# Optimization experiments

Hardware: AMD Instinct MI355X
Metric: run time of the kernel (lower is better)

Reference implementation:

```python
import jax, jax.numpy as jnp
import numpy as np

P = 16        # patch size
WIN = 64      # attention window size
NH = 12       # num heads


def _layernorm(x, g, b, eps=1e-5):
    m = x.mean(-1, keepdims=True)
    v = ((x - m) ** 2).mean(-1, keepdims=True)
    return (x - m) * jax.lax.rsqrt(v + eps) * g + b


def _sinusoidal_pe(n, d):
    pos = jnp.arange(n, dtype=jnp.float32)[:, None]
    i = jnp.arange(d // 2, dtype=jnp.float32)[None, :]
    ang = pos / jnp.power(10000.0, (2.0 * i) / d)
    pe = jnp.zeros((n, d), jnp.float32)
    pe = pe.at[:, 0::2].set(jnp.sin(ang)).at[:, 1::2].set(jnp.cos(ang))
    return pe


def setup_inputs() -> dict:
    key = jax.random.key(0)
    ks = jax.random.split(key, 8)
    B, C, H, W, D, F = 16, 3, 512, 512, 768, 3072
    s = lambda k, shape: (jax.random.normal(k, shape, jnp.float32) * 0.02)
    return {
        "input": jax.random.normal(ks[0], (B, C, H, W), jnp.float32),
        "patch_w": s(ks[1], (D, C, P, P)),
        "patch_b": jnp.zeros((D,), jnp.float32),
        "ln_g": jnp.ones((D,), jnp.float32),
        "ln_b": jnp.zeros((D,), jnp.float32),
        "qkv_w": s(ks[2], (D, 3 * D)),
        "qkv_b": jnp.zeros((3 * D,), jnp.float32),
        "proj_w": s(ks[3], (D, D)),
        "proj_b": jnp.zeros((D,), jnp.float32),
        "ff1_w": s(ks[4], (D, F)),
        "ff1_b": jnp.zeros((F,), jnp.float32),
        "ff2_w": s(ks[5], (F, D)),
        "ff2_b": jnp.zeros((D,), jnp.float32),
    }


def reference(input, patch_w, patch_b, ln_g, ln_b, qkv_w, qkv_b,
              proj_w, proj_b, ff1_w, ff1_b, ff2_w, ff2_b):
    B, C, H, W = input.shape
    D = patch_w.shape[0]
    dh = D // NH
    # --- patch embedding (conv k=stride=P as einsum) + norm ---
    xp = input.reshape(B, C, H // P, P, W // P, P)
    x = jnp.einsum('bchpwq,dcpq->bhwd', xp, patch_w) + patch_b  # [B,32,32,D]
    x = x.reshape(B, -1, D)                                      # [B,N,D]
    x = _layernorm(x, ln_g, ln_b)
    N = x.shape[1]
    # --- static sinusoidal position embedding ---
    x = x + _sinusoidal_pe(N, D)

    def ff(y):  # shared feedforward (dropout=eval/off)
        return jax.nn.gelu(y @ ff1_w + ff1_b) @ ff2_w + ff2_b

    def sparse_attn(y):  # windowed block-sparse attention, window=64
        nW = N // WIN
        qkv = (y @ qkv_w + qkv_b).reshape(B, nW, WIN, 3, NH, dh)
        q, k, v = qkv[:, :, :, 0], qkv[:, :, :, 1], qkv[:, :, :, 2]
        scores = jnp.einsum('bwqhd,bwkhd->bwhqk', q, k) * (dh ** -0.5)
        a = jax.nn.softmax(scores, axis=-1)
        o = jnp.einsum('bwhqk,bwkhd->bwqhd', a, v).reshape(B, N, D)
        return o @ proj_w + proj_b

    identity = x
    x = ff(x)
    x = sparse_attn(x)
    x = x + identity
    identity = x
    x = ff(x)
    x = x + identity
    return x
```

## Files before the change

### kernel.cpp

```cpp
#include <hip/hip_runtime.h>

typedef unsigned int uint;
typedef short bf16x8 __attribute__((ext_vector_type(8)));
typedef float f32x4 __attribute__((ext_vector_type(4)));

__device__ __forceinline__ unsigned short f2b(float f) {
    uint u = __builtin_bit_cast(uint, f);
    u += 0x7fffu + ((u >> 16) & 1u);
    return (unsigned short)(u >> 16);
}
__device__ __forceinline__ float b2f(unsigned short h) {
    uint u = ((uint)h) << 16;
    return __builtin_bit_cast(float, u);
}

__device__ __forceinline__ float fast_gelu(float v) {
    float s  = v * v;
    float t2 = __builtin_fmaf(0.044715f * s, v, v);
    float e  = __expf(-1.5957691216f * t2);
    return v * __builtin_amdgcn_rcpf(1.0f + e);
}

__device__ __forceinline__ void gl_lds16(const unsigned short* g, unsigned short* l) {
    __builtin_amdgcn_global_load_lds(
        reinterpret_cast<const __attribute__((address_space(1))) unsigned int*>(
            reinterpret_cast<uintptr_t>(g)),
        reinterpret_cast<__attribute__((address_space(3))) unsigned int*>(
            reinterpret_cast<uintptr_t>(l)),
        16, 0, 0);
}

__global__ __launch_bounds__(256) void convert_bf16_kernel(const float* __restrict__ src,
                                                           unsigned short* __restrict__ dst, int n) {
    int idx = blockIdx.x * 256 + threadIdx.x;
    if (idx < n) dst[idx] = f2b(src[idx]);
}

__global__ __launch_bounds__(256) void transpose_to_bf16_kernel(const float* __restrict__ src,
                                                                unsigned short* __restrict__ dst,
                                                                int K, int N) {
    long long idx = (long long)blockIdx.x * 256 + threadIdx.x;
    if (idx >= (long long)K * N) return;
    int k = (int)(idx / N);
    int n = (int)(idx % N);
    dst[(long long)n * K + k] = f2b(src[idx]);
}

__global__ __launch_bounds__(256) void im2col_kernel(const float* __restrict__ in,
                                                     unsigned short* __restrict__ out) {
    long long idx = (long long)blockIdx.x * 256 + threadIdx.x;
    int k = (int)(idx % 768);
    int n = (int)(idx / 768);
    int b = n >> 10, t = n & 1023;
    int hp = t >> 5, wp = t & 31;
    int c = k >> 8, rm = k & 255;
    int p = rm >> 4, q = rm & 15;
    long long src = (((long long)(b * 3 + c) * 512) + hp * 16 + p) * 512 + wp * 16 + q;
    out[idx] = f2b(in[src]);
}

__global__ __launch_bounds__(256) void ln_pe_kernel(const float* __restrict__ xe,
                                                    const float* __restrict__ g,
                                                    const float* __restrict__ bb,
                                                    unsigned short* __restrict__ xb) {
    int row = blockIdx.x;
    int pos = row & 1023;
    const float* xr = xe + (long long)row * 768;
    float v0 = xr[threadIdx.x];
    float v1 = xr[threadIdx.x + 256];
    float v2 = xr[threadIdx.x + 512];
    float s = v0 + v1 + v2;
    float sq = v0 * v0 + v1 * v1 + v2 * v2;
    for (int o = 32; o > 0; o >>= 1) {
        s  += __shfl_down(s, o, 64);
        sq += __shfl_down(sq, o, 64);
    }
    __shared__ float ps[4], pq[4];
    int w = threadIdx.x >> 6, lane = threadIdx.x & 63;
    if (lane == 0) { ps[w] = s; pq[w] = sq; }
    __syncthreads();
    float ts = ps[0] + ps[1] + ps[2] + ps[3];
    float tq = pq[0] + pq[1] + pq[2] + pq[3];
    float mean = ts * (1.0f / 768.0f);
    float var  = tq * (1.0f / 768.0f) - mean * mean;
    float inv  = rsqrtf(var + 1e-5f);
    #pragma unroll
    for (int dd = 0; dd < 3; dd++) {
        int d = threadIdx.x + dd * 256;
        float val = (dd == 0) ? v0 : (dd == 1) ? v1 : v2;
        float y = (val - mean) * inv * g[d] + bb[d];
        float freq = __expf(-(float)(d & ~1) * (9.210340371976184f / 768.0f));
        float ang = (float)pos * freq;
        y += (d & 1) ? cosf(ang) : sinf(ang);
        xb[(long long)row * 768 + d] = f2b(y);
    }
}

__global__ __launch_bounds__(256) void gemm128_kernel(const unsigned short* __restrict__ A,
                                                      const unsigned short* __restrict__ BT,
                                                      const float* __restrict__ bias,
                                                      const unsigned short* __restrict__ residB,
                                                      float* __restrict__ outF,
                                                      unsigned short* __restrict__ outB,
                                                      int M, int N, int K, int ldb,
                                                      int epi, int accumF) {
    __shared__ unsigned short As[128 * 64];
    __shared__ unsigned short Bs[128 * 64];

    const int nX = N >> 7;
    int id = blockIdx.x;
    int xcd = id & 7;
    int sq_ = id >> 3;
    int bx = sq_ % nX;
    int by = (sq_ / nX) * 8 + xcd;

    const int tid = threadIdx.x;
    const int m0 = by * 128, n0 = bx * 128;
    const int w = tid >> 6, lane = tid & 63;
    const int wm = (w >> 1) * 64, wn = (w & 1) * 64;
    const int quad = lane >> 4, l15 = lane & 15;

    const int srow = tid >> 3;
    const int sc8  = tid & 7;
    const int gc8  = sc8 ^ (srow & 7);
    const unsigned short* Ag0 = A  + (long long)(m0 + srow) * K + gc8 * 8;
    const unsigned short* Ag1 = Ag0 + (long long)32 * K;
    const unsigned short* Ag2 = Ag0 + (long long)64 * K;
    const unsigned short* Ag3 = Ag0 + (long long)96 * K;
    const unsigned short* Bg0 = BT + (long long)(n0 + srow) * ldb + gc8 * 8;
    const unsigned short* Bg1 = Bg0 + (long long)32 * ldb;
    const unsigned short* Bg2 = Bg0 + (long long)64 * ldb;
    const unsigned short* Bg3 = Bg0 + (long long)96 * ldb;
    unsigned short* Ad0 = As + srow * 64 + sc8 * 8;
    unsigned short* Ad1 = Ad0 + 32 * 64;
    unsigned short* Ad2 = Ad0 + 64 * 64;
    unsigned short* Ad3 = Ad0 + 96 * 64;
    unsigned short* Bd0 = Bs + srow * 64 + sc8 * 8;
    unsigned short* Bd1 = Bd0 + 32 * 64;
    unsigned short* Bd2 = Bd0 + 64 * 64;
    unsigned short* Bd3 = Bd0 + 96 * 64;

    f32x4 acc[4][4] = {};
    const int swz = l15 & 7;

    for (int k0 = 0; k0 < K; k0 += 64) {
        __syncthreads();
        gl_lds16(Ag0 + k0, Ad0);
        gl_lds16(Ag1 + k0, Ad1);
        gl_lds16(Ag2 + k0, Ad2);
        gl_lds16(Ag3 + k0, Ad3);
        gl_lds16(Bg0 + k0, Bd0);
        gl_lds16(Bg1 + k0, Bd1);
        gl_lds16(Bg2 + k0, Bd2);
        gl_lds16(Bg3 + k0, Bd3);
        __syncthreads();

        #pragma unroll
        for (int h = 0; h < 2; h++) {
            const int c8 = h * 4 + quad;
            bf16x8 af[4], bfr[4];
            #pragma unroll
            for (int i = 0; i < 4; i++)
                af[i] = *(const bf16x8*)(As + (wm + i * 16 + l15) * 64 + ((c8 ^ swz) * 8));
            #pragma unroll
            for (int j = 0; j < 4; j++)
                bfr[j] = *(const bf16x8*)(Bs + (wn + j * 16 + l15) * 64 + ((c8 ^ swz) * 8));
            #pragma unroll
            for (int i = 0; i < 4; i++)
                #pragma unroll
                for (int j = 0; j < 4; j++)
                    acc[i][j] = __builtin_amdgcn_mfma_f32_16x16x32_bf16(af[i], bfr[j], acc[i][j], 0, 0, 0);
        }
    }

    const int r0 = quad * 4;
    #pragma unroll
    for (int i = 0; i < 4; i++) {
        #pragma unroll
        for (int j = 0; j < 4; j++) {
            int gn = n0 + wn + j * 16 + l15;
            float bv = bias ? bias[gn] : 0.0f;
            #pragma unroll
            for (int r = 0; r < 4; r++) {
                int gm = m0 + wm + i * 16 + r0 + r;
                float v = acc[i][j][r] + bv;
                if (epi == 1) v = fast_gelu(v);
                long long off = (long long)gm * N + gn;
                if (accumF) v += outF[off];
                if (residB) v += b2f(residB[off]);
                if (outF) outF[off] = v;
                if (outB) outB[off] = f2b(v);
            }
        }
    }
}

__global__ __launch_bounds__(256) void attn_kernel(const unsigned short* __restrict__ qkv,
                                                   unsigned short* __restrict__ o) {
    __shared__ float qs[64 * 65], ks[64 * 65], vs[64 * 65];
    __shared__ float pmax[4 * 64], psum[4 * 64];
    int blk = blockIdx.x;
    int h = blk % 12;
    int bw = blk / 12;
    int wi = bw % 16, b = bw / 16;
    int rowBase = b * 1024 + wi * 64;
    int tid = threadIdx.x;

    int lr = tid >> 2, c0 = (tid & 3) * 16;
    const unsigned short* src = qkv + (long long)(rowBase + lr) * 2304 + h * 64 + c0;
    #pragma unroll
    for (int j = 0; j < 16; j++) {
        qs[lr * 65 + c0 + j] = b2f(src[j]);
        ks[lr * 65 + c0 + j] = b2f(src[768 + j]);
        vs[lr * 65 + c0 + j] = b2f(src[1536 + j]);
    }
    __syncthreads();

    int r = tid & 63, cg = tid >> 6;
    float svals[16] = {};
    for (int kk = 0; kk < 64; kk++) {
        float qv = qs[r * 65 + kk];
        #pragma unroll
        for (int j = 0; j < 16; j++)
            svals[j] += qv * ks[(cg * 16 + j) * 65 + kk];
    }
    float smax = -1e30f;
    #pragma unroll
    for (int j = 0; j < 16; j++) {
        svals[j] *= 0.125f;
        smax = fmaxf(smax, svals[j]);
    }
    pmax[cg * 64 + r] = smax;
    __syncthreads();
    float m = fmaxf(fmaxf(pmax[r], pmax[64 + r]), fmaxf(pmax[128 + r], pmax[192 + r]));
    float lsum = 0.0f;
    #pragma unroll
    for (int j = 0; j < 16; j++) {
        float e = __expf(svals[j] - m);
        qs[r * 65 + cg * 16 + j] = e;
        lsum += e;
    }
    psum[cg * 64 + r] = lsum;
    __syncthreads();
    float inv = __builtin_amdgcn_rcpf(psum[r] + psum[64 + r] + psum[128 + r] + psum[192 + r]);

    float oacc[16] = {};
    for (int c = 0; c < 64; c++) {
        float pv = qs[r * 65 + c];
        #pragma unroll
        for (int j = 0; j < 16; j++)
            oacc[j] += pv * vs[c * 65 + cg * 16 + j];
    }
    unsigned short* dst = o + (long long)(rowBase + r) * 768 + h * 64 + cg * 16;
    #pragma unroll
    for (int j = 0; j < 16; j++) dst[j] = f2b(oacc[j] * inv);
}

extern "C" void kernel_launch(void* const* d_in, const int* in_sizes, int n_in,
                              void* d_out, int out_size, void* d_ws, size_t ws_size,
                              hipStream_t stream) {
    const float* input   = (const float*)d_in[0];
    const float* patch_w = (const float*)d_in[1];
    const float* patch_b = (const float*)d_in[2];
    const float* ln_g    = (const float*)d_in[3];
    const float* ln_b    = (const float*)d_in[4];
    const float* qkv_w   = (const float*)d_in[5];
    const float* qkv_b   = (const float*)d_in[6];
    const float* proj_w  = (const float*)d_in[7];
    const float* proj_b  = (const float*)d_in[8];
    const float* ff1_w   = (const float*)d_in[9];
    const float* ff1_b   = (const float*)d_in[10];
    const float* ff2_w   = (const float*)d_in[11];
    const float* ff2_b   = (const float*)d_in[12];
    float* out = (float*)d_out;

    const int MN = 16384;
    const int D = 768, F = 3072, TD = 2304;
    const int NY = MN / 128;

    unsigned short* wPatch = (unsigned short*)d_ws;
    unsigned short* wQkvT  = wPatch + 589824;
    unsigned short* wProjT = wQkvT + 1769472;
    unsigned short* wFf1T  = wProjT + 589824;
    unsigned short* wFf2T  = wFf1T + 2359296;
    unsigned short* bigBuf = wFf2T + 2359296;
    unsigned short* xid    = bigBuf + 50331648;
    unsigned short* t0     = xid + 12582912;

    convert_bf16_kernel<<<(589824 + 255) / 256, 256, 0, stream>>>(patch_w, wPatch, 589824);
    transpose_to_bf16_kernel<<<(1769472 + 255) / 256, 256, 0, stream>>>(qkv_w, wQkvT, D, TD);
    transpose_to_bf16_kernel<<<(589824 + 255) / 256, 256, 0, stream>>>(proj_w, wProjT, D, D);
    transpose_to_bf16_kernel<<<(2359296 + 255) / 256, 256, 0, stream>>>(ff1_w, wFf1T, D, F);
    transpose_to_bf16_kernel<<<(2359296 + 255) / 256, 256, 0, stream>>>(ff2_w, wFf2T, F, D);

    im2col_kernel<<<(MN * 768) / 256, 256, 0, stream>>>(input, bigBuf);

    gemm128_kernel<<<(D / 128) * NY, 256, 0, stream>>>(bigBuf, wPatch, patch_b, nullptr,
                                                       out, nullptr, MN, D, 768, 768, 0, 0);
    ln_pe_kernel<<<MN, 256, 0, stream>>>(out, ln_g, ln_b, xid);

    gemm128_kernel<<<(F / 128) * NY, 256, 0, stream>>>(xid, wFf1T, ff1_b, nullptr,
                                                       nullptr, bigBuf, MN, F, 768, 768, 1, 0);
    gemm128_kernel<<<(D / 128) * NY, 256, 0, stream>>>(bigBuf, wFf2T, ff2_b, nullptr,
                                                       nullptr, t0, MN, D, F, F, 0, 0);
    gemm128_kernel<<<(TD / 128) * NY, 256, 0, stream>>>(t0, wQkvT, qkv_b, nullptr,
                                                        nullptr, bigBuf, MN, TD, 768, 768, 0, 0);
    attn_kernel<<<16 * 16 * 12, 256, 0, stream>>>(bigBuf, t0);

    gemm128_kernel<<<(D / 128) * NY, 256, 0, stream>>>(t0, wProjT, proj_b, xid,
                                                       nullptr, xid, MN, D, 768, 768, 0, 0);

    gemm128_kernel<<<(F / 128) * NY, 256, 0, stream>>>(xid, wFf1T, ff1_b, nullptr,
                                                       nullptr, bigBuf, MN, F, 768, 768, 1, 0);
    gemm128_kernel<<<(D / 128) * NY, 256, 0, stream>>>(bigBuf, wFf2T, ff2_b, xid,
                                                       out, nullptr, MN, D, F, F, 0, 0);
}
```

Measured before the change: 900.1 us.

## Replace 128x128 GEMM with double-buffered 256x256 tile, 8-wave pipelined kernel

```diff
diff --git a/kernel.cpp b/kernel.cpp
--- a/kernel.cpp
+++ b/kernel.cpp
@@ -96,7 +96,7 @@
     }
 }
 
-__global__ __launch_bounds__(256) void gemm128_kernel(const unsigned short* __restrict__ A,
+__global__ __launch_bounds__(512) void gemm256_kernel(const unsigned short* __restrict__ A,
                                                       const unsigned short* __restrict__ BT,
                                                       const float* __restrict__ bias,
                                                       const unsigned short* __restrict__ residB,
@@ -104,95 +104,141 @@
                                                       unsigned short* __restrict__ outB,
                                                       int M, int N, int K, int ldb,
                                                       int epi, int accumF) {
-    __shared__ unsigned short As[128 * 64];
-    __shared__ unsigned short Bs[128 * 64];
-
-    const int nX = N >> 7;
+    __shared__ __align__(16) unsigned short As[2][256 * 64];
+    __shared__ __align__(16) unsigned short Bs[2][256 * 64];
+
+    const int nX = N >> 8;
     int id = blockIdx.x;
     int xcd = id & 7;
     int sq_ = id >> 3;
     int bx = sq_ % nX;
     int by = (sq_ / nX) * 8 + xcd;
+    const int m0 = by * 256, n0 = bx * 256;
 
     const int tid = threadIdx.x;
-    const int m0 = by * 128, n0 = bx * 128;
     const int w = tid >> 6, lane = tid & 63;
-    const int wm = (w >> 1) * 64, wn = (w & 1) * 64;
+    const int wr = w >> 2, wc = w & 3;
     const int quad = lane >> 4, l15 = lane & 15;
-
-    const int srow = tid >> 3;
-    const int sc8  = tid & 7;
-    const int gc8  = sc8 ^ (srow & 7);
-    const unsigned short* Ag0 = A  + (long long)(m0 + srow) * K + gc8 * 8;
-    const unsigned short* Ag1 = Ag0 + (long long)32 * K;
-    const unsigned short* Ag2 = Ag0 + (long long)64 * K;
-    const unsigned short* Ag3 = Ag0 + (long long)96 * K;
-    const unsigned short* Bg0 = BT + (long long)(n0 + srow) * ldb + gc8 * 8;
-    const unsigned short* Bg1 = Bg0 + (long long)32 * ldb;
-    const unsigned short* Bg2 = Bg0 + (long long)64 * ldb;
-    const unsigned short* Bg3 = Bg0 + (long long)96 * ldb;
-    unsigned short* Ad0 = As + srow * 64 + sc8 * 8;
-    unsigned short* Ad1 = Ad0 + 32 * 64;
-    unsigned short* Ad2 = Ad0 + 64 * 64;
-    unsigned short* Ad3 = Ad0 + 96 * 64;
-    unsigned short* Bd0 = Bs + srow * 64 + sc8 * 8;
-    unsigned short* Bd1 = Bd0 + 32 * 64;
-    unsigned short* Bd2 = Bd0 + 64 * 64;
-    unsigned short* Bd3 = Bd0 + 96 * 64;
-
-    f32x4 acc[4][4] = {};
     const int swz = l15 & 7;
 
-    for (int k0 = 0; k0 < K; k0 += 64) {
-        __syncthreads();
-        gl_lds16(Ag0 + k0, Ad0);
-        gl_lds16(Ag1 + k0, Ad1);
-        gl_lds16(Ag2 + k0, Ad2);
-        gl_lds16(Ag3 + k0, Ad3);
-        gl_lds16(Bg0 + k0, Bd0);
-        gl_lds16(Bg1 + k0, Bd1);
-        gl_lds16(Bg2 + k0, Bd2);
-        gl_lds16(Bg3 + k0, Bd3);
-        __syncthreads();
-
+    const int row0 = tid >> 3;
+    const int c8   = tid & 7;
+    const int gc8  = c8 ^ (row0 & 7);
+    const unsigned short* Ag = A  + (long long)(m0 + row0) * K   + gc8 * 8;
+    const unsigned short* Bg = BT + (long long)(n0 + row0) * ldb + gc8 * 8;
+    unsigned short* Ad = &As[0][0] + row0 * 64 + c8 * 8;
+    unsigned short* Bd = &Bs[0][0] + row0 * 64 + c8 * 8;
+    const long long aK64 = (long long)64 * K,  aK128 = (long long)128 * K;
+    const long long bL64 = (long long)64 * ldb, bL128 = (long long)128 * ldb;
+
+#define STAGE_A(bsel, h, ks) { \
+    const unsigned short* s_ = Ag + (h) * aK128 + (ks); \
+    unsigned short* d_ = Ad + (bsel) * 16384 + (h) * 8192; \
+    gl_lds16(s_, d_); gl_lds16(s_ + aK64, d_ + 4096); }
+#define STAGE_B(bsel, h, ks) { \
+    const unsigned short* s_ = Bg + (h) * bL128 + (ks); \
+    unsigned short* d_ = Bd + (bsel) * 16384 + (h) * 8192; \
+    gl_lds16(s_, d_); gl_lds16(s_ + bL64, d_ + 4096); }
+
+    bf16x8 af[4][2], bfr[2][2];
+    f32x4 acc[2][2][4][2] = {};
+
+#define LOAD_AF(bsel, qm) { \
+    const unsigned short* base_ = &As[bsel][((qm) * 128 + wr * 64 + l15) * 64]; \
+    _Pragma("unroll") for (int mf_ = 0; mf_ < 4; mf_++) { \
+      af[mf_][0] = *(const bf16x8*)(base_ + mf_ * 1024 + ((quad ^ swz) * 8)); \
+      af[mf_][1] = *(const bf16x8*)(base_ + mf_ * 1024 + (((4 + quad) ^ swz) * 8)); \
+    } }
+#define LOAD_BF(bsel, qn) { \
+    const unsigned short* base_ = &Bs[bsel][((qn) * 128 + wc * 32 + l15) * 64]; \
+    _Pragma("unroll") for (int nf_ = 0; nf_ < 2; nf_++) { \
+      bfr[nf_][0] = *(const bf16x8*)(base_ + nf_ * 1024 + ((quad ^ swz) * 8)); \
+      bfr[nf_][1] = *(const bf16x8*)(base_ + nf_ * 1024 + (((4 + quad) ^ swz) * 8)); \
+    } }
+#define MFMA_Q(qm, qn) { \
+    __builtin_amdgcn_sched_barrier(0); \
+    __builtin_amdgcn_s_setprio(1); \
+    _Pragma("unroll") for (int mf_ = 0; mf_ < 4; mf_++) \
+    _Pragma("unroll") for (int nf_ = 0; nf_ < 2; nf_++) { \
+      acc[qm][qn][mf_][nf_] = __builtin_amdgcn_mfma_f32_16x16x32_bf16(af[mf_][0], bfr[nf_][0], acc[qm][qn][mf_][nf_], 0, 0, 0); \
+      acc[qm][qn][mf_][nf_] = __builtin_amdgcn_mfma_f32_16x16x32_bf16(af[mf_][1], bfr[nf_][1], acc[qm][qn][mf_][nf_], 0, 0, 0); \
+    } \
+    __builtin_amdgcn_s_setprio(0); \
+    __builtin_amdgcn_sched_barrier(0); }
+#define BAR() { asm volatile("" ::: "memory"); __builtin_amdgcn_s_barrier(); asm volatile("" ::: "memory"); }
+
+    const int NT = K >> 6;
+
+    STAGE_B(0, 0, 0);
+    STAGE_A(0, 0, 0);
+    STAGE_B(0, 1, 0);
+    STAGE_A(0, 1, 0);
+    STAGE_A(1, 0, 64);
+    STAGE_B(1, 1, 64);
+    STAGE_A(1, 1, 64);
+    asm volatile("s_waitcnt vmcnt(6)" ::: "memory");
+    BAR();
+
+    for (int s = 0; s < NT; s++) {
+        const int b = s & 1, bn = b ^ 1;
+        const int ks1 = (s + 1 < NT) ? (s + 1) * 64 : 0;
+        const int ks2 = (s + 2 < NT) ? (s + 2) * 64 : 0;
+
+        LOAD_AF(b, 0);
+        LOAD_BF(b, 0);
+        STAGE_B(bn, 0, ks1);
+        asm volatile("s_waitcnt lgkmcnt(8)" ::: "memory");
+        BAR();
+        MFMA_Q(0, 0);
+        BAR();
+        LOAD_BF(b, 1);
+        STAGE_A(b, 0, ks2);
+        BAR();
+        MFMA_Q(0, 1);
+        BAR();
+        LOAD_AF(b, 1);
+        STAGE_B(b, 1, ks2);
+        BAR();
+        MFMA_Q(1, 1);
+        BAR();
+        LOAD_BF(b, 0);
+        STAGE_A(b, 1, ks2);
+        BAR();
+        MFMA_Q(1, 0);
+        asm volatile("s_waitcnt vmcnt(6)" ::: "memory");
+        BAR();
+    }
+    asm volatile("s_waitcnt vmcnt(0)" ::: "memory");
+
+    const int r0 = quad * 4;
+    #pragma unroll
+    for (int qm = 0; qm < 2; qm++)
+    #pragma unroll
+    for (int qn = 0; qn < 2; qn++)
+    #pragma unroll
+    for (int mf = 0; mf < 4; mf++)
+    #pragma unroll
+    for (int nf = 0; nf < 2; nf++) {
+        int gn = n0 + qn * 128 + wc * 32 + nf * 16 + l15;
+        float bv = bias ? bias[gn] : 0.0f;
         #pragma unroll
-        for (int h = 0; h < 2; h++) {
-            const int c8 = h * 4 + quad;
-            bf16x8 af[4], bfr[4];
-            #pragma unroll
-            for (int i = 0; i < 4; i++)
-                af[i] = *(const bf16x8*)(As + (wm + i * 16 + l15) * 64 + ((c8 ^ swz) * 8));
-            #pragma unroll
-            for (int j = 0; j < 4; j++)
-                bfr[j] = *(const bf16x8*)(Bs + (wn + j * 16 + l15) * 64 + ((c8 ^ swz) * 8));
-            #pragma unroll
-            for (int i = 0; i < 4; i++)
-                #pragma unroll
-                for (int j = 0; j < 4; j++)
-                    acc[i][j] = __builtin_amdgcn_mfma_f32_16x16x32_bf16(af[i], bfr[j], acc[i][j], 0, 0, 0);
+        for (int r = 0; r < 4; r++) {
+            int gm = m0 + qm * 128 + wr * 64 + mf * 16 + r0 + r;
+            float v = acc[qm][qn][mf][nf][r] + bv;
+            if (epi == 1) v = fast_gelu(v);
+            long long off = (long long)gm * N + gn;
+            if (accumF) v += outF[off];
+            if (residB) v += b2f(residB[off]);
+            if (outF) outF[off] = v;
+            if (outB) outB[off] = f2b(v);
         }
     }
-
-    const int r0 = quad * 4;
-    #pragma unroll
-    for (int i = 0; i < 4; i++) {
-        #pragma unroll
-        for (int j = 0; j < 4; j++) {
-            int gn = n0 + wn + j * 16 + l15;
-            float bv = bias ? bias[gn] : 0.0f;
-            #pragma unroll
-            for (int r = 0; r < 4; r++) {
-                int gm = m0 + wm + i * 16 + r0 + r;
-                float v = acc[i][j][r] + bv;
-                if (epi == 1) v = fast_gelu(v);
-                long long off = (long long)gm * N + gn;
-                if (accumF) v += outF[off];
-                if (residB) v += b2f(residB[off]);
-                if (outF) outF[off] = v;
-                if (outB) outB[off] = f2b(v);
-            }
-        }
-    }
+#undef STAGE_A
+#undef STAGE_B
+#undef LOAD_AF
+#undef LOAD_BF
+#undef MFMA_Q
+#undef BAR
 }
 
 __global__ __launch_bounds__(256) void attn_kernel(const unsigned short* __restrict__ qkv,
@@ -276,7 +322,7 @@
 
     const int MN = 16384;
     const int D = 768, F = 3072, TD = 2304;
-    const int NY = MN / 128;
+    const int NY = MN / 256;
 
     unsigned short* wPatch = (unsigned short*)d_ws;
     unsigned short* wQkvT  = wPatch + 589824;
@@ -295,23 +341,23 @@
 
     im2col_kernel<<<(MN * 768) / 256, 256, 0, stream>>>(input, bigBuf);
 
-    gemm128_kernel<<<(D / 128) * NY, 256, 0, stream>>>(bigBuf, wPatch, patch_b, nullptr,
+    gemm256_kernel<<<(D / 256) * NY, 512, 0, stream>>>(bigBuf, wPatch, patch_b, nullptr,
                                                        out, nullptr, MN, D, 768, 768, 0, 0);
     ln_pe_kernel<<<MN, 256, 0, stream>>>(out, ln_g, ln_b, xid);
 
-    gemm128_kernel<<<(F / 128) * NY, 256, 0, stream>>>(xid, wFf1T, ff1_b, nullptr,
+    gemm256_kernel<<<(F / 256) * NY, 512, 0, stream>>>(xid, wFf1T, ff1_b, nullptr,
                                                        nullptr, bigBuf, MN, F, 768, 768, 1, 0);
-    gemm128_kernel<<<(D / 128) * NY, 256, 0, stream>>>(bigBuf, wFf2T, ff2_b, nullptr,
+    gemm256_kernel<<<(D / 256) * NY, 512, 0, stream>>>(bigBuf, wFf2T, ff2_b, nullptr,
                                                        nullptr, t0, MN, D, F, F, 0, 0);
-    gemm128_kernel<<<(TD / 128) * NY, 256, 0, stream>>>(t0, wQkvT, qkv_b, nullptr,
+    gemm256_kernel<<<(TD / 256) * NY, 512, 0, stream>>>(t0, wQkvT, qkv_b, nullptr,
                                                         nullptr, bigBuf, MN, TD, 768, 768, 0, 0);
     attn_kernel<<<16 * 16 * 12, 256, 0, stream>>>(bigBuf, t0);
 
-    gemm128_kernel<<<(D / 128) * NY, 256, 0, stream>>>(t0, wProjT, proj_b, xid,
+    gemm256_kernel<<<(D / 256) * NY, 512, 0, stream>>>(t0, wProjT, proj_b, xid,
                                                        nullptr, xid, MN, D, 768, 768, 0, 0);
 
-    gemm128_kernel<<<(F / 128) * NY, 256, 0, stream>>>(xid, wFf1T, ff1_b, nullptr,
+    gemm256_kernel<<<(F / 256) * NY, 512, 0, stream>>>(xid, wFf1T, ff1_b, nullptr,
                                                        nullptr, bigBuf, MN, F, 768, 768, 1, 0);
-    gemm128_kernel<<<(D / 128) * NY, 256, 0, stream>>>(bigBuf, wFf2T, ff2_b, xid,
+    gemm256_kernel<<<(D / 256) * NY, 512, 0, stream>>>(bigBuf, wFf2T, ff2_b, xid,
                                                        out, nullptr, MN, D, F, F, 0, 0);
 }
```

Result: slower. 940.0 us (+4.4%).

## Load GEMM MFMA fragments directly from global memory with register double buffering

Applied to the files above, without the earlier changes.

```diff
diff --git a/kernel.cpp b/kernel.cpp
--- a/kernel.cpp
+++ b/kernel.cpp
@@ -19,15 +19,6 @@
     float t2 = __builtin_fmaf(0.044715f * s, v, v);
     float e  = __expf(-1.5957691216f * t2);
     return v * __builtin_amdgcn_rcpf(1.0f + e);
-}
-
-__device__ __forceinline__ void gl_lds16(const unsigned short* g, unsigned short* l) {
-    __builtin_amdgcn_global_load_lds(
-        reinterpret_cast<const __attribute__((address_space(1))) unsigned int*>(
-            reinterpret_cast<uintptr_t>(g)),
-        reinterpret_cast<__attribute__((address_space(3))) unsigned int*>(
-            reinterpret_cast<uintptr_t>(l)),
-        16, 0, 0);
 }
 
 __global__ __launch_bounds__(256) void convert_bf16_kernel(const float* __restrict__ src,
@@ -96,82 +87,57 @@
     }
 }
 
-__global__ __launch_bounds__(256) void gemm128_kernel(const unsigned short* __restrict__ A,
-                                                      const unsigned short* __restrict__ BT,
-                                                      const float* __restrict__ bias,
-                                                      const unsigned short* __restrict__ residB,
-                                                      float* __restrict__ outF,
-                                                      unsigned short* __restrict__ outB,
-                                                      int M, int N, int K, int ldb,
-                                                      int epi, int accumF) {
-    __shared__ unsigned short As[128 * 64];
-    __shared__ unsigned short Bs[128 * 64];
-
+__global__ __launch_bounds__(256) void gemm128d_kernel(const unsigned short* __restrict__ A,
+                                                       const unsigned short* __restrict__ BT,
+                                                       const float* __restrict__ bias,
+                                                       const unsigned short* __restrict__ residB,
+                                                       float* __restrict__ outF,
+                                                       unsigned short* __restrict__ outB,
+                                                       int M, int N, int K, int ldb,
+                                                       int epi, int accumF) {
     const int nX = N >> 7;
     int id = blockIdx.x;
     int xcd = id & 7;
     int sq_ = id >> 3;
     int bx = sq_ % nX;
     int by = (sq_ / nX) * 8 + xcd;
+    const int m0 = by * 128, n0 = bx * 128;
 
     const int tid = threadIdx.x;
-    const int m0 = by * 128, n0 = bx * 128;
     const int w = tid >> 6, lane = tid & 63;
     const int wm = (w >> 1) * 64, wn = (w & 1) * 64;
     const int quad = lane >> 4, l15 = lane & 15;
 
-    const int srow = tid >> 3;
-    const int sc8  = tid & 7;
-    const int gc8  = sc8 ^ (srow & 7);
-    const unsigned short* Ag0 = A  + (long long)(m0 + srow) * K + gc8 * 8;
-    const unsigned short* Ag1 = Ag0 + (long long)32 * K;
-    const unsigned short* Ag2 = Ag0 + (long long)64 * K;
-    const unsigned short* Ag3 = Ag0 + (long long)96 * K;
-    const unsigned short* Bg0 = BT + (long long)(n0 + srow) * ldb + gc8 * 8;
-    const unsigned short* Bg1 = Bg0 + (long long)32 * ldb;
-    const unsigned short* Bg2 = Bg0 + (long long)64 * ldb;
-    const unsigned short* Bg3 = Bg0 + (long long)96 * ldb;
-    unsigned short* Ad0 = As + srow * 64 + sc8 * 8;
-    unsigned short* Ad1 = Ad0 + 32 * 64;
-    unsigned short* Ad2 = Ad0 + 64 * 64;
-    unsigned short* Ad3 = Ad0 + 96 * 64;
-    unsigned short* Bd0 = Bs + srow * 64 + sc8 * 8;
-    unsigned short* Bd1 = Bd0 + 32 * 64;
-    unsigned short* Bd2 = Bd0 + 64 * 64;
-    unsigned short* Bd3 = Bd0 + 96 * 64;
+    const long long lK = K, lL = ldb;
+    const unsigned short* Ar = A  + (long long)(m0 + wm + l15) * lK + quad * 8;
+    const unsigned short* Br = BT + (long long)(n0 + wn + l15) * lL + quad * 8;
 
     f32x4 acc[4][4] = {};
-    const int swz = l15 & 7;
-
-    for (int k0 = 0; k0 < K; k0 += 64) {
-        __syncthreads();
-        gl_lds16(Ag0 + k0, Ad0);
-        gl_lds16(Ag1 + k0, Ad1);
-        gl_lds16(Ag2 + k0, Ad2);
-        gl_lds16(Ag3 + k0, Ad3);
-        gl_lds16(Bg0 + k0, Bd0);
-        gl_lds16(Bg1 + k0, Bd1);
-        gl_lds16(Bg2 + k0, Bd2);
-        gl_lds16(Bg3 + k0, Bd3);
-        __syncthreads();
-
-        #pragma unroll
-        for (int h = 0; h < 2; h++) {
-            const int c8 = h * 4 + quad;
-            bf16x8 af[4], bfr[4];
-            #pragma unroll
-            for (int i = 0; i < 4; i++)
-                af[i] = *(const bf16x8*)(As + (wm + i * 16 + l15) * 64 + ((c8 ^ swz) * 8));
-            #pragma unroll
-            for (int j = 0; j < 4; j++)
-                bfr[j] = *(const bf16x8*)(Bs + (wn + j * 16 + l15) * 64 + ((c8 ^ swz) * 8));
-            #pragma unroll
-            for (int i = 0; i < 4; i++)
-                #pragma unroll
-                for (int j = 0; j < 4; j++)
-                    acc[i][j] = __builtin_amdgcn_mfma_f32_16x16x32_bf16(af[i], bfr[j], acc[i][j], 0, 0, 0);
-        }
-    }
+    bf16x8 a0[4], b0[4], a1[4], b1[4];
+
+#define LD(Aset, Bset, kk) { \
+    _Pragma("unroll") for (int i = 0; i < 4; i++) \
+        Aset[i] = *(const bf16x8*)(Ar + (long long)i * 16 * lK + (kk)); \
+    _Pragma("unroll") for (int j = 0; j < 4; j++) \
+        Bset[j] = *(const bf16x8*)(Br + (long long)j * 16 * lL + (kk)); }
+#define FM(Aset, Bset) { \
+    _Pragma("unroll") for (int i = 0; i < 4; i++) \
+    _Pragma("unroll") for (int j = 0; j < 4; j++) \
+        acc[i][j] = __builtin_amdgcn_mfma_f32_16x16x32_bf16(Aset[i], Bset[j], acc[i][j], 0, 0, 0); }
+
+    const int KS = K >> 5;
+    LD(a0, b0, 0);
+    for (int ks = 0; ks + 2 < KS; ks += 2) {
+        LD(a1, b1, (ks + 1) * 32);
+        FM(a0, b0);
+        LD(a0, b0, (ks + 2) * 32);
+        FM(a1, b1);
+    }
+    LD(a1, b1, (KS - 1) * 32);
+    FM(a0, b0);
+    FM(a1, b1);
+#undef LD
+#undef FM
 
     const int r0 = quad * 4;
     #pragma unroll
@@ -295,23 +261,23 @@
 
     im2col_kernel<<<(MN * 768) / 256, 256, 0, stream>>>(input, bigBuf);
 
-    gemm128_kernel<<<(D / 128) * NY, 256, 0, stream>>>(bigBuf, wPatch, patch_b, nullptr,
-                                                       out, nullptr, MN, D, 768, 768, 0, 0);
+    gemm128d_kernel<<<(D / 128) * NY, 256, 0, stream>>>(bigBuf, wPatch, patch_b, nullptr,
+                                                        out, nullptr, MN, D, 768, 768, 0, 0);
     ln_pe_kernel<<<MN, 256, 0, stream>>>(out, ln_g, ln_b, xid);
 
-    gemm128_kernel<<<(F / 128) * NY, 256, 0, stream>>>(xid, wFf1T, ff1_b, nullptr,
-                                                       nullptr, bigBuf, MN, F, 768, 768, 1, 0);
-    gemm128_kernel<<<(D / 128) * NY, 256, 0, stream>>>(bigBuf, wFf2T, ff2_b, nullptr,
-                                                       nullptr, t0, MN, D, F, F, 0, 0);
-    gemm128_kernel<<<(TD / 128) * NY, 256, 0, stream>>>(t0, wQkvT, qkv_b, nullptr,
-                                                        nullptr, bigBuf, MN, TD, 768, 768, 0, 0);
+    gemm128d_kernel<<<(F / 128) * NY, 256, 0, stream>>>(xid, wFf1T, ff1_b, nullptr,
+                                                        nullptr, bigBuf, MN, F, 768, 768, 1, 0);
+    gemm128d_kernel<<<(D / 128) * NY, 256, 0, stream>>>(bigBuf, wFf2T, ff2_b, nullptr,
+                                                        nullptr, t0, MN, D, F, F, 0, 0);
+    gemm128d_kernel<<<(TD / 128) * NY, 256, 0, stream>>>(t0, wQkvT, qkv_b, nullptr,
+                                                         nullptr, bigBuf, MN, TD, 768, 768, 0, 0);
     attn_kernel<<<16 * 16 * 12, 256, 0, stream>>>(bigBuf, t0);
 
-    gemm128_kernel<<<(D / 128) * NY, 256, 0, stream>>>(t0, wProjT, proj_b, xid,
-                                                       nullptr, xid, MN, D, 768, 768, 0, 0);
-
-    gemm128_kernel<<<(F / 128) * NY, 256, 0, stream>>>(xid, wFf1T, ff1_b, nullptr,
-                                                       nullptr, bigBuf, MN, F, 768, 768, 1, 0);
-    gemm128_kernel<<<(D / 128) * NY, 256, 0, stream>>>(bigBuf, wFf2T, ff2_b, xid,
-                                                       out, nullptr, MN, D, F, F, 0, 0);
-}
+    gemm128d_kernel<<<(D / 128) * NY, 256, 0, stream>>>(t0, wProjT, proj_b, xid,
+                                                        nullptr, xid, MN, D, 768, 768, 0, 0);
+
+    gemm128d_kernel<<<(F / 128) * NY, 256, 0, stream>>>(xid, wFf1T, ff1_b, nullptr,
+                                                        nullptr, bigBuf, MN, F, 768, 768, 1, 0);
+    gemm128d_kernel<<<(D / 128) * NY, 256, 0, stream>>>(bigBuf, wFf2T, ff2_b, xid,
+                                                        out, nullptr, MN, D, F, F, 0, 0);
+}
```

New measurement: 2.014 ms. +123.7%, slower.
